# Kernel tuning notes

Measured on AMD Instinct MI355X. Metric: run time of the kernel, lower is better.

The kernel has to match this reference:

```python
import jax, jax.numpy as jnp
import numpy as np

N_NODES = 100000
N_EDGES = 3200000
D_FEAT = 64


def setup_inputs() -> dict:
    key = jax.random.key(0)
    k_x, k_r, k_c, k_v = jax.random.split(key, 4)
    x = jax.random.normal(k_x, (N_NODES, D_FEAT), dtype=jnp.float32)
    edge_row = jax.random.randint(k_r, (N_EDGES,), 0, N_NODES, dtype=jnp.int64)
    edge_col = jax.random.randint(k_c, (N_EDGES,), 0, N_NODES, dtype=jnp.int64)
    # positive values mimicking symmetric-normalized adjacency weights
    edge_val = jax.random.uniform(k_v, (N_EDGES,), dtype=jnp.float32)
    t = jnp.zeros((1,), dtype=jnp.float32)  # ODE time, unused by this linear GCN step
    return {"t": t, "x": x, "edge_row": edge_row, "edge_col": edge_col, "edge_val": edge_val}


def reference(t, x, edge_row, edge_col, edge_val):
    # out = A_sparse @ x, COO SpMM as gather -> scale -> segment-sum scatter
    # gathered: [n_edges, d]
    gathered = edge_val[:, None] * x[edge_col]
    out = jax.ops.segment_sum(gathered, edge_row, num_segments=N_NODES)
    return out
```

## Files before the change

### kernel.cpp

```cpp
#include <hip/hip_runtime.h>
#include <hip/hip_bf16.h>
#include <hip/hip_fp16.h>

#define D 64
#define RB 128
#define NB_MAX 1024
#define NBLK1 512
#define P1CAP 6272
#define CAP 5120

typedef unsigned long long ull;
typedef unsigned short u16;

__device__ __forceinline__ ull pack_rec(float v, int r, int c) {
    return ((ull)__float_as_uint(v) << 32) |
           (ull)(((unsigned)(r & (RB - 1)) << 17) | (unsigned)c);
}

__global__ __launch_bounds__(256) void spmm_atomic_kernel(
    const float* __restrict__ x,
    const int*   __restrict__ edge_row,
    const int*   __restrict__ edge_col,
    const float* __restrict__ edge_val,
    float*       __restrict__ out,
    int n_edges)
{
    const int gtid = blockIdx.x * blockDim.x + threadIdx.x;
    const int wave = gtid >> 6;
    const int lane = threadIdx.x & 63;
    if (wave >= n_edges) return;
    const int   r = edge_row[wave];
    const int   c = edge_col[wave];
    const float v = edge_val[wave];
    atomicAdd(&out[(size_t)r * D + lane], v * x[(size_t)c * D + lane]);
}

__global__ __launch_bounds__(256) void p1_localsort_kernel(
    const int* __restrict__ rows, const int* __restrict__ cols,
    const float* __restrict__ vals,
    ull* __restrict__ staged, u16* __restrict__ counts, u16* __restrict__ startpos,
    int n_edges, int nb, int chunk)
{
    __shared__ ull stage[P1CAP];
    __shared__ int cnt[NB_MAX];
    __shared__ int s[256];
    const int t = threadIdx.x, blk = blockIdx.x;
    const int e0 = blk * chunk;
    const int e1 = min(e0 + chunk, n_edges);
    const int len = e1 - e0;

    for (int i = t; i < nb; i += 256) cnt[i] = 0;
    __syncthreads();

    for (int i = e0 + t * 4; i < e1; i += 1024) {
        if (i + 4 <= e1) {
            const int4 r4 = *(const int4*)(rows + i);
            atomicAdd(&cnt[r4.x >> 7], 1);
            atomicAdd(&cnt[r4.y >> 7], 1);
            atomicAdd(&cnt[r4.z >> 7], 1);
            atomicAdd(&cnt[r4.w >> 7], 1);
        } else {
            for (int k = i; k < e1; ++k) atomicAdd(&cnt[rows[k] >> 7], 1);
        }
    }
    __syncthreads();

    int pre[4], sum = 0;
    const int base = t * 4;
    #pragma unroll
    for (int k = 0; k < 4; ++k) {
        const int idx = base + k;
        const int c = (idx < nb) ? cnt[idx] : 0;
        if (idx < nb) counts[(size_t)idx * NBLK1 + blk] = (u16)c;
        pre[k] = sum; sum += c;
    }
    s[t] = sum;
    for (int off = 1; off < 256; off <<= 1) {
        __syncthreads();
        const int w = (t >= off) ? s[t - off] : 0;
        __syncthreads();
        s[t] += w;
    }
    const int texcl = s[t] - sum;
    __syncthreads();
    #pragma unroll
    for (int k = 0; k < 4; ++k) {
        const int idx = base + k;
        if (idx < nb) {
            const int e = texcl + pre[k];
            cnt[idx] = e;
            startpos[(size_t)idx * NBLK1 + blk] = (u16)e;
        }
    }
    __syncthreads();

    for (int i = e0 + t * 4; i < e1; i += 1024) {
        if (i + 4 <= e1) {
            const int4   r4 = *(const int4*)(rows + i);
            const int4   c4 = *(const int4*)(cols + i);
            const float4 v4 = *(const float4*)(vals + i);
            int p;
            p = atomicAdd(&cnt[r4.x >> 7], 1); stage[p] = pack_rec(v4.x, r4.x, c4.x);
            p = atomicAdd(&cnt[r4.y >> 7], 1); stage[p] = pack_rec(v4.y, r4.y, c4.y);
            p = atomicAdd(&cnt[r4.z >> 7], 1); stage[p] = pack_rec(v4.z, r4.z, c4.z);
            p = atomicAdd(&cnt[r4.w >> 7], 1); stage[p] = pack_rec(v4.w, r4.w, c4.w);
        } else {
            for (int k = i; k < e1; ++k) {
                const int p = atomicAdd(&cnt[rows[k] >> 7], 1);
                stage[p] = pack_rec(vals[k], rows[k], cols[k]);
            }
        }
    }
    __syncthreads();

    for (int i = t; i < len; i += 256)
        staged[(size_t)blk * chunk + i] = stage[i];
}

__global__ __launch_bounds__(256) void p2_binsum_kernel(
    const u16* __restrict__ counts, int* __restrict__ binsum, int nb)
{
    __shared__ int s[256];
    const int b = blockIdx.x, t = threadIdx.x;
    const int acc = (int)counts[(size_t)b * NBLK1 + t] +
                    (int)counts[(size_t)b * NBLK1 + t + 256];
    s[t] = acc;
    __syncthreads();
    for (int off = 128; off > 0; off >>= 1) {
        if (t < off) s[t] += s[t + off];
        __syncthreads();
    }
    if (t == 0) binsum[b] = s[0];
}

__global__ __launch_bounds__(1024) void p3_scanbins_kernel(
    const int* __restrict__ binsum, int* __restrict__ binbase,
    int* __restrict__ flags, int nb)
{
    __shared__ int s[1024];
    const int t = threadIdx.x;
    const int mine = (t < nb) ? binsum[t] : 0;
    s[t] = mine;
    for (int off = 1; off < 1024; off <<= 1) {
        __syncthreads();
        const int v = (t >= off) ? s[t - off] : 0;
        __syncthreads();
        s[t] += v;
    }
    if (t < nb) { binbase[t] = s[t] - mine; flags[t] = 0; }
    if (t == nb - 1) binbase[nb] = s[t];
}

__global__ __launch_bounds__(256) void p4_binsort_kernel(
    const ull* __restrict__ staged, const u16* __restrict__ counts,
    const u16* __restrict__ startpos, const int* __restrict__ binbase,
    ull* __restrict__ recs, int* __restrict__ offsets_row, int* __restrict__ flags,
    int nb, int n_nodes, int chunk)
{
    __shared__ ull stage[CAP];
    __shared__ int doff[NBLK1 + 1];
    __shared__ int srcs[NBLK1];
    __shared__ int cnt[1024];
    __shared__ int s[256];
    const int b = blockIdx.x, t = threadIdx.x;
    const int s0 = binbase[b];

    const int la = (int)counts[(size_t)b * NBLK1 + 2 * t];
    const int lb = (int)counts[(size_t)b * NBLK1 + 2 * t + 1];
    srcs[2 * t]     = (int)startpos[(size_t)b * NBLK1 + 2 * t];
    srcs[2 * t + 1] = (int)startpos[(size_t)b * NBLK1 + 2 * t + 1];
    const int mysum = la + lb;
    s[t] = mysum;
    for (int off = 1; off < 256; off <<= 1) {
        __syncthreads();
        const int w = (t >= off) ? s[t - off] : 0;
        __syncthreads();
        s[t] += w;
    }
    const int excl = s[t] - mysum;
    doff[2 * t] = excl;
    doff[2 * t + 1] = excl + la;
    if (t == 255) doff[NBLK1] = s[255];
    __syncthreads();
    const int len = doff[NBLK1];

    if (len > CAP) {
        if (t == 0) flags[b] = 1;
        for (int i = t; i < len; i += 256) {
            int lo = 0, hi = NBLK1 - 1;
            while (lo < hi) {
                const int mid = (lo + hi + 1) >> 1;
                if (doff[mid] <= i) lo = mid; else hi = mid - 1;
            }
            recs[s0 + i] = staged[(size_t)lo * chunk + srcs[lo] + (i - doff[lo])];
        }
        if (t == 0 && b * RB <= n_nodes) offsets_row[b * RB] = s0;
        return;
    }

    for (int i = t; i < 1024; i += 256) cnt[i] = 0;
    __syncthreads();

    for (int i = t; i < len; i += 256) {
        int lo = 0, hi = NBLK1 - 1;
        while (lo < hi) {
            const int mid = (lo + hi + 1) >> 1;
            if (doff[mid] <= i) lo = mid; else hi = mid - 1;
        }
        const ull rr = staged[(size_t)lo * chunk + srcs[lo] + (i - doff[lo])];
        stage[i] = rr;
        const int key = ((int)((rr >> 17) & (RB - 1)) << 3) |
                        (int)(((unsigned)rr & 0x1FFFF) >> 14);
        atomicAdd(&cnt[key], 1);
    }
    __syncthreads();

    int v[4], pre[4], sum = 0;
    const int base = t * 4;
    #pragma unroll
    for (int k = 0; k < 4; ++k) { v[k] = cnt[base + k]; pre[k] = sum; sum += v[k]; }
    s[t] = sum;
    for (int off = 1; off < 256; off <<= 1) {
        __syncthreads();
        const int w = (t >= off) ? s[t - off] : 0;
        __syncthreads();
        s[t] += w;
    }
    const int texcl = s[t] - sum;
    __syncthreads();
    #pragma unroll
    for (int k = 0; k < 4; ++k) cnt[base + k] = texcl + pre[k];
    __syncthreads();

    if (t <= RB) {
        const int r = b * RB + t;
        if (r <= n_nodes)
            offsets_row[r] = s0 + ((t == RB) ? len : cnt[t << 3]);
    }
    __syncthreads();

    for (int i = t; i < len; i += 256) {
        const ull rr = stage[i];
        const int key = ((int)((rr >> 17) & (RB - 1)) << 3) |
                        (int)(((unsigned)rr & 0x1FFFF) >> 14);
        const int p = atomicAdd(&cnt[key], 1);
        recs[s0 + p] = rr;
    }
}

__global__ void tohalf_kernel(const float* __restrict__ x,
                              __half2* __restrict__ xh2, int n4)
{
    for (int i = blockIdx.x * blockDim.x + threadIdx.x; i < n4;
         i += gridDim.x * blockDim.x) {
        const float4 v = ((const float4*)x)[i];
        xh2[2 * i + 0] = __floats2half2_rn(v.x, v.y);
        xh2[2 * i + 1] = __floats2half2_rn(v.z, v.w);
    }
}

__global__ __launch_bounds__(256, 8) void spmm_csr_half2_kernel(
    const __half* __restrict__ xh,
    const int*   __restrict__ offsets_row,
    const int*   __restrict__ binbase,
    const ull*   __restrict__ recs,
    const int*   __restrict__ flags,
    float*       __restrict__ out,
    int n_nodes)
{
    const int row  = blockIdx.x * 4 + (threadIdx.x >> 6);
    if (row >= n_nodes) return;
    const int lane = threadIdx.x & 63;
    const int b    = row >> 7;

    if (__builtin_expect(flags[b], 0)) {
        float acc = 0.f;
        const int s  = binbase[b];
        const int e  = binbase[b + 1];
        const int lr = row & (RB - 1);
        for (int j = s; j < e; ++j) {
            const ull rec = recs[j];
            if ((int)((rec >> 17) & (RB - 1)) == lr) {
                const int   c = (int)((unsigned)rec & 0x1FFFF);
                const float v = __uint_as_float((unsigned)(rec >> 32));
                acc += v * __half2float(xh[(size_t)c * D + lane]);
            }
        }
        out[(size_t)row * D + lane] = acc;
        return;
    }

    const __half2* xh2 = (const __half2*)xh;
    const int half = lane >> 5;
    const int fl   = lane & 31;

    const int s = offsets_row[row];
    const int e = offsets_row[row + 1];
    float accx = 0.f, accy = 0.f;

    int j = s;
    for (; j + 16 <= e; j += 16) {
        float vv[8]; int aa[8];
        #pragma unroll
        for (int k = 0; k < 8; ++k) {
            const ull rec = recs[j + 2 * k + half];
            vv[k] = __uint_as_float((unsigned)(rec >> 32));
            aa[k] = ((int)((unsigned)rec & 0x1FFFF) << 5) + fl;
        }
        __half2 hv[8];
        #pragma unroll
        for (int k = 0; k < 8; ++k) hv[k] = xh2[aa[k]];
        __builtin_amdgcn_sched_barrier(0);
        #pragma unroll
        for (int k = 0; k < 8; ++k) {
            const float2 xf = __half22float2(hv[k]);
            accx = fmaf(vv[k], xf.x, accx);
            accy = fmaf(vv[k], xf.y, accy);
        }
    }
    if (j < e) {
        const int safe = e - 1;
        float vv[8]; int aa[8];
        #pragma unroll
        for (int k = 0; k < 8; ++k) {
            const int  idx = j + 2 * k + half;
            const bool ok  = idx < e;
            const ull  rec = recs[ok ? idx : safe];
            vv[k] = ok ? __uint_as_float((unsigned)(rec >> 32)) : 0.f;
            aa[k] = ((int)((unsigned)rec & 0x1FFFF) << 5) + fl;
        }
        __half2 hv[8];
        #pragma unroll
        for (int k = 0; k < 8; ++k) hv[k] = xh2[aa[k]];
        __builtin_amdgcn_sched_barrier(0);
        #pragma unroll
        for (int k = 0; k < 8; ++k) {
            const float2 xf = __half22float2(hv[k]);
            accx = fmaf(vv[k], xf.x, accx);
            accy = fmaf(vv[k], xf.y, accy);
        }
    }

    accx += __shfl_xor(accx, 32);
    accy += __shfl_xor(accy, 32);
    if (half == 0) {
        float2 o; o.x = accx; o.y = accy;
        ((float2*)out)[(size_t)row * 32 + fl] = o;
    }
}

static inline size_t align16(size_t v) { return (v + 15) & ~(size_t)15; }

extern "C" void kernel_launch(void* const* d_in, const int* in_sizes, int n_in,
                              void* d_out, int out_size, void* d_ws, size_t ws_size,
                              hipStream_t stream)
{
    const float* x        = (const float*)d_in[1];
    const int*   edge_row = (const int*)d_in[2];
    const int*   edge_col = (const int*)d_in[3];
    const float* edge_val = (const float*)d_in[4];
    float*       out      = (float*)d_out;

    const int n_edges = in_sizes[2];
    const int n_nodes = out_size / D;
    const int nb      = (n_nodes + RB - 1) / RB;
    const int chunk   = (((n_edges + NBLK1 - 1) / NBLK1) + 3) & ~3;

    const size_t off_recs    = 0;
    const size_t off_staged  = align16(off_recs + (size_t)n_edges * 8);
    const size_t off_counts  = align16(off_staged + (size_t)NBLK1 * chunk * 8);
    const size_t off_start   = align16(off_counts + (size_t)nb * NBLK1 * 2);
    const size_t off_binsum  = align16(off_start + (size_t)nb * NBLK1 * 2);
    const size_t off_binbase = align16(off_binsum + (size_t)nb * 4);
    const size_t off_rowoffs = align16(off_binbase + (size_t)(nb + 1) * 4);
    const size_t off_flags   = align16(off_rowoffs + (size_t)(n_nodes + 1) * 4);
    const size_t ws_needed   = off_flags + (size_t)nb * 4;
    const size_t xh_bytes    = (size_t)n_nodes * D * 2;

    if (ws_size < ws_needed || nb > NB_MAX || n_nodes > (1 << 17) ||
        chunk > P1CAP || xh_bytes > (size_t)NBLK1 * chunk * 8) {
        hipMemsetAsync(out, 0, (size_t)out_size * sizeof(float), stream);
        const int n_blocks = (n_edges + 3) / 4;
        spmm_atomic_kernel<<<n_blocks, 256, 0, stream>>>(
            x, edge_row, edge_col, edge_val, out, n_edges);
        return;
    }

    char* ws = (char*)d_ws;
    ull*    recs        = (ull*)(ws + off_recs);
    ull*    staged      = (ull*)(ws + off_staged);
    u16*    counts      = (u16*)(ws + off_counts);
    u16*    startpos    = (u16*)(ws + off_start);
    int*    binsum      = (int*)(ws + off_binsum);
    int*    binbase     = (int*)(ws + off_binbase);
    int*    offsets_row = (int*)(ws + off_rowoffs);
    int*    flags       = (int*)(ws + off_flags);
    __half* xh          = (__half*)(ws + off_staged);

    p1_localsort_kernel<<<NBLK1, 256, 0, stream>>>(
        edge_row, edge_col, edge_val, staged, counts, startpos,
        n_edges, nb, chunk);
    p2_binsum_kernel<<<nb, 256, 0, stream>>>(counts, binsum, nb);
    p3_scanbins_kernel<<<1, 1024, 0, stream>>>(binsum, binbase, flags, nb);
    p4_binsort_kernel<<<nb, 256, 0, stream>>>(
        staged, counts, startpos, binbase, recs, offsets_row, flags,
        nb, n_nodes, chunk);
    const int n4 = (n_nodes * D) / 4;
    tohalf_kernel<<<2048, 256, 0, stream>>>(x, (__half2*)xh, n4);
    spmm_csr_half2_kernel<<<(n_nodes + 3) / 4, 256, 0, stream>>>(
        xh, offsets_row, binbase, recs, flags, out, n_nodes);
}
```

Before: 259.1 us.

## Scatter locally sorted edges straight to global bin positions, drop staging buffer

```diff
diff --git a/kernel.cpp b/kernel.cpp
--- a/kernel.cpp
+++ b/kernel.cpp
@@ -35,19 +35,14 @@
     atomicAdd(&out[(size_t)r * D + lane], v * x[(size_t)c * D + lane]);
 }
 
-__global__ __launch_bounds__(256) void p1_localsort_kernel(
-    const int* __restrict__ rows, const int* __restrict__ cols,
-    const float* __restrict__ vals,
-    ull* __restrict__ staged, u16* __restrict__ counts, u16* __restrict__ startpos,
+__global__ __launch_bounds__(256) void p1a_hist_kernel(
+    const int* __restrict__ rows, u16* __restrict__ counts,
     int n_edges, int nb, int chunk)
 {
-    __shared__ ull stage[P1CAP];
     __shared__ int cnt[NB_MAX];
-    __shared__ int s[256];
     const int t = threadIdx.x, blk = blockIdx.x;
     const int e0 = blk * chunk;
     const int e1 = min(e0 + chunk, n_edges);
-    const int len = e1 - e0;
 
     for (int i = t; i < nb; i += 256) cnt[i] = 0;
     __syncthreads();
@@ -65,14 +60,75 @@
     }
     __syncthreads();
 
-    int pre[4], sum = 0;
+    for (int i = t; i < nb; i += 256)
+        counts[(size_t)i * NBLK1 + blk] = (u16)cnt[i];
+}
+
+__global__ __launch_bounds__(256) void p2_scanblocks_kernel(
+    const u16* __restrict__ counts, int* __restrict__ dest32,
+    int* __restrict__ binsum, int nb)
+{
+    __shared__ int s[256];
+    const int b = blockIdx.x, t = threadIdx.x;
+    const int la = (int)counts[(size_t)b * NBLK1 + 2 * t];
+    const int lb = (int)counts[(size_t)b * NBLK1 + 2 * t + 1];
+    const int mysum = la + lb;
+    s[t] = mysum;
+    for (int off = 1; off < 256; off <<= 1) {
+        __syncthreads();
+        const int w = (t >= off) ? s[t - off] : 0;
+        __syncthreads();
+        s[t] += w;
+    }
+    const int excl = s[t] - mysum;
+    dest32[(size_t)b * NBLK1 + 2 * t]     = excl;
+    dest32[(size_t)b * NBLK1 + 2 * t + 1] = excl + la;
+    if (t == 255) binsum[b] = s[255];
+}
+
+__global__ __launch_bounds__(1024) void p3_scanbins_kernel(
+    const int* __restrict__ binsum, int* __restrict__ binbase,
+    int* __restrict__ flags, int nb)
+{
+    __shared__ int s[1024];
+    const int t = threadIdx.x;
+    const int mine = (t < nb) ? binsum[t] : 0;
+    s[t] = mine;
+    for (int off = 1; off < 1024; off <<= 1) {
+        __syncthreads();
+        const int v = (t >= off) ? s[t - off] : 0;
+        __syncthreads();
+        s[t] += v;
+    }
+    if (t < nb) { binbase[t] = s[t] - mine; flags[t] = 0; }
+    if (t == nb - 1) binbase[nb] = s[t];
+}
+
+__global__ __launch_bounds__(256) void p1b_sortwrite_kernel(
+    const int* __restrict__ rows, const int* __restrict__ cols,
+    const float* __restrict__ vals,
+    const u16* __restrict__ counts, const int* __restrict__ dest32,
+    const int* __restrict__ binbase,
+    ull* __restrict__ recs, int n_edges, int nb, int chunk)
+{
+    __shared__ ull stage[P1CAP];
+    __shared__ u16 binof[P1CAP];
+    __shared__ int cnt[NB_MAX];
+    __shared__ u16 doffL[NB_MAX];
+    __shared__ int gbase[NB_MAX];
+    __shared__ int s[256];
+    const int t = threadIdx.x, blk = blockIdx.x;
+    const int e0 = blk * chunk;
+    const int e1 = min(e0 + chunk, n_edges);
+    const int len = e1 - e0;
+
+    int pre[4], sum = 0, c4[4];
     const int base = t * 4;
     #pragma unroll
     for (int k = 0; k < 4; ++k) {
         const int idx = base + k;
-        const int c = (idx < nb) ? cnt[idx] : 0;
-        if (idx < nb) counts[(size_t)idx * NBLK1 + blk] = (u16)c;
-        pre[k] = sum; sum += c;
+        c4[k] = (idx < nb) ? (int)counts[(size_t)idx * NBLK1 + blk] : 0;
+        pre[k] = sum; sum += c4[k];
     }
     s[t] = sum;
     for (int off = 1; off < 256; off <<= 1) {
@@ -88,8 +144,9 @@
         const int idx = base + k;
         if (idx < nb) {
             const int e = texcl + pre[k];
-            cnt[idx] = e;
-            startpos[(size_t)idx * NBLK1 + blk] = (u16)e;
+            cnt[idx]   = e;
+            doffL[idx] = (u16)e;
+            gbase[idx] = binbase[idx] + dest32[(size_t)idx * NBLK1 + blk];
         }
     }
     __syncthreads();
@@ -97,104 +154,47 @@
     for (int i = e0 + t * 4; i < e1; i += 1024) {
         if (i + 4 <= e1) {
             const int4   r4 = *(const int4*)(rows + i);
-            const int4   c4 = *(const int4*)(cols + i);
+            const int4   c4v = *(const int4*)(cols + i);
             const float4 v4 = *(const float4*)(vals + i);
             int p;
-            p = atomicAdd(&cnt[r4.x >> 7], 1); stage[p] = pack_rec(v4.x, r4.x, c4.x);
-            p = atomicAdd(&cnt[r4.y >> 7], 1); stage[p] = pack_rec(v4.y, r4.y, c4.y);
-            p = atomicAdd(&cnt[r4.z >> 7], 1); stage[p] = pack_rec(v4.z, r4.z, c4.z);
-            p = atomicAdd(&cnt[r4.w >> 7], 1); stage[p] = pack_rec(v4.w, r4.w, c4.w);
+            p = atomicAdd(&cnt[r4.x >> 7], 1); stage[p] = pack_rec(v4.x, r4.x, c4v.x); binof[p] = (u16)(r4.x >> 7);
+            p = atomicAdd(&cnt[r4.y >> 7], 1); stage[p] = pack_rec(v4.y, r4.y, c4v.y); binof[p] = (u16)(r4.y >> 7);
+            p = atomicAdd(&cnt[r4.z >> 7], 1); stage[p] = pack_rec(v4.z, r4.z, c4v.z); binof[p] = (u16)(r4.z >> 7);
+            p = atomicAdd(&cnt[r4.w >> 7], 1); stage[p] = pack_rec(v4.w, r4.w, c4v.w); binof[p] = (u16)(r4.w >> 7);
         } else {
             for (int k = i; k < e1; ++k) {
                 const int p = atomicAdd(&cnt[rows[k] >> 7], 1);
                 stage[p] = pack_rec(vals[k], rows[k], cols[k]);
+                binof[p] = (u16)(rows[k] >> 7);
             }
         }
     }
     __syncthreads();
 
-    for (int i = t; i < len; i += 256)
-        staged[(size_t)blk * chunk + i] = stage[i];
-}
-
-__global__ __launch_bounds__(256) void p2_binsum_kernel(
-    const u16* __restrict__ counts, int* __restrict__ binsum, int nb)
-{
-    __shared__ int s[256];
-    const int b = blockIdx.x, t = threadIdx.x;
-    const int acc = (int)counts[(size_t)b * NBLK1 + t] +
-                    (int)counts[(size_t)b * NBLK1 + t + 256];
-    s[t] = acc;
-    __syncthreads();
-    for (int off = 128; off > 0; off >>= 1) {
-        if (t < off) s[t] += s[t + off];
-        __syncthreads();
-    }
-    if (t == 0) binsum[b] = s[0];
-}
-
-__global__ __launch_bounds__(1024) void p3_scanbins_kernel(
-    const int* __restrict__ binsum, int* __restrict__ binbase,
-    int* __restrict__ flags, int nb)
-{
-    __shared__ int s[1024];
-    const int t = threadIdx.x;
-    const int mine = (t < nb) ? binsum[t] : 0;
-    s[t] = mine;
-    for (int off = 1; off < 1024; off <<= 1) {
-        __syncthreads();
-        const int v = (t >= off) ? s[t - off] : 0;
-        __syncthreads();
-        s[t] += v;
-    }
-    if (t < nb) { binbase[t] = s[t] - mine; flags[t] = 0; }
-    if (t == nb - 1) binbase[nb] = s[t];
-}
-
-__global__ __launch_bounds__(256) void p4_binsort_kernel(
-    const ull* __restrict__ staged, const u16* __restrict__ counts,
-    const u16* __restrict__ startpos, const int* __restrict__ binbase,
+    for (int i = t; i < len; i += 256) {
+        const int bin = (int)binof[i];
+        const int g   = gbase[bin] + (i - (int)doffL[bin]);
+        recs[g] = stage[i];
+    }
+}
+
+__global__ __launch_bounds__(256) void p4_sortbin_kernel(
+    const int* __restrict__ binbase,
     ull* __restrict__ recs, int* __restrict__ offsets_row, int* __restrict__ flags,
-    int nb, int n_nodes, int chunk)
+    int n_nodes)
 {
     __shared__ ull stage[CAP];
-    __shared__ int doff[NBLK1 + 1];
-    __shared__ int srcs[NBLK1];
     __shared__ int cnt[1024];
     __shared__ int s[256];
     const int b = blockIdx.x, t = threadIdx.x;
-    const int s0 = binbase[b];
-
-    const int la = (int)counts[(size_t)b * NBLK1 + 2 * t];
-    const int lb = (int)counts[(size_t)b * NBLK1 + 2 * t + 1];
-    srcs[2 * t]     = (int)startpos[(size_t)b * NBLK1 + 2 * t];
-    srcs[2 * t + 1] = (int)startpos[(size_t)b * NBLK1 + 2 * t + 1];
-    const int mysum = la + lb;
-    s[t] = mysum;
-    for (int off = 1; off < 256; off <<= 1) {
-        __syncthreads();
-        const int w = (t >= off) ? s[t - off] : 0;
-        __syncthreads();
-        s[t] += w;
-    }
-    const int excl = s[t] - mysum;
-    doff[2 * t] = excl;
-    doff[2 * t + 1] = excl + la;
-    if (t == 255) doff[NBLK1] = s[255];
-    __syncthreads();
-    const int len = doff[NBLK1];
+    const int s0  = binbase[b];
+    const int len = binbase[b + 1] - s0;
 
     if (len > CAP) {
-        if (t == 0) flags[b] = 1;
-        for (int i = t; i < len; i += 256) {
-            int lo = 0, hi = NBLK1 - 1;
-            while (lo < hi) {
-                const int mid = (lo + hi + 1) >> 1;
-                if (doff[mid] <= i) lo = mid; else hi = mid - 1;
-            }
-            recs[s0 + i] = staged[(size_t)lo * chunk + srcs[lo] + (i - doff[lo])];
-        }
-        if (t == 0 && b * RB <= n_nodes) offsets_row[b * RB] = s0;
+        if (t == 0) {
+            flags[b] = 1;
+            if (b * RB <= n_nodes) offsets_row[b * RB] = s0;
+        }
         return;
     }
 
@@ -202,12 +202,7 @@
     __syncthreads();
 
     for (int i = t; i < len; i += 256) {
-        int lo = 0, hi = NBLK1 - 1;
-        while (lo < hi) {
-            const int mid = (lo + hi + 1) >> 1;
-            if (doff[mid] <= i) lo = mid; else hi = mid - 1;
-        }
-        const ull rr = staged[(size_t)lo * chunk + srcs[lo] + (i - doff[lo])];
+        const ull rr = recs[s0 + i];
         stage[i] = rr;
         const int key = ((int)((rr >> 17) & (RB - 1)) << 3) |
                         (int)(((unsigned)rr & 0x1FFFF) >> 14);
@@ -367,18 +362,17 @@
     const int chunk   = (((n_edges + NBLK1 - 1) / NBLK1) + 3) & ~3;
 
     const size_t off_recs    = 0;
-    const size_t off_staged  = align16(off_recs + (size_t)n_edges * 8);
-    const size_t off_counts  = align16(off_staged + (size_t)NBLK1 * chunk * 8);
-    const size_t off_start   = align16(off_counts + (size_t)nb * NBLK1 * 2);
-    const size_t off_binsum  = align16(off_start + (size_t)nb * NBLK1 * 2);
+    const size_t off_xh      = align16(off_recs + (size_t)n_edges * 8);
+    const size_t off_counts  = align16(off_xh + (size_t)n_nodes * D * 2);
+    const size_t off_dest    = align16(off_counts + (size_t)nb * NBLK1 * 2);
+    const size_t off_binsum  = align16(off_dest + (size_t)nb * NBLK1 * 4);
     const size_t off_binbase = align16(off_binsum + (size_t)nb * 4);
     const size_t off_rowoffs = align16(off_binbase + (size_t)(nb + 1) * 4);
     const size_t off_flags   = align16(off_rowoffs + (size_t)(n_nodes + 1) * 4);
     const size_t ws_needed   = off_flags + (size_t)nb * 4;
-    const size_t xh_bytes    = (size_t)n_nodes * D * 2;
 
     if (ws_size < ws_needed || nb > NB_MAX || n_nodes > (1 << 17) ||
-        chunk > P1CAP || xh_bytes > (size_t)NBLK1 * chunk * 8) {
+        chunk > P1CAP || n_edges < 1) {
         hipMemsetAsync(out, 0, (size_t)out_size * sizeof(float), stream);
         const int n_blocks = (n_edges + 3) / 4;
         spmm_atomic_kernel<<<n_blocks, 256, 0, stream>>>(
@@ -388,23 +382,23 @@
 
     char* ws = (char*)d_ws;
     ull*    recs        = (ull*)(ws + off_recs);
-    ull*    staged      = (ull*)(ws + off_staged);
+    __half* xh          = (__half*)(ws + off_xh);
     u16*    counts      = (u16*)(ws + off_counts);
-    u16*    startpos    = (u16*)(ws + off_start);
+    int*    dest32      = (int*)(ws + off_dest);
     int*    binsum      = (int*)(ws + off_binsum);
     int*    binbase     = (int*)(ws + off_binbase);
     int*    offsets_row = (int*)(ws + off_rowoffs);
     int*    flags       = (int*)(ws + off_flags);
-    __half* xh          = (__half*)(ws + off_staged);
-
-    p1_localsort_kernel<<<NBLK1, 256, 0, stream>>>(
-        edge_row, edge_col, edge_val, staged, counts, startpos,
-        n_edges, nb, chunk);
-    p2_binsum_kernel<<<nb, 256, 0, stream>>>(counts, binsum, nb);
+
+    p1a_hist_kernel<<<NBLK1, 256, 0, stream>>>(
+        edge_row, counts, n_edges, nb, chunk);
+    p2_scanblocks_kernel<<<nb, 256, 0, stream>>>(counts, dest32, binsum, nb);
     p3_scanbins_kernel<<<1, 1024, 0, stream>>>(binsum, binbase, flags, nb);
-    p4_binsort_kernel<<<nb, 256, 0, stream>>>(
-        staged, counts, startpos, binbase, recs, offsets_row, flags,
-        nb, n_nodes, chunk);
+    p1b_sortwrite_kernel<<<NBLK1, 256, 0, stream>>>(
+        edge_row, edge_col, edge_val, counts, dest32, binbase,
+        recs, n_edges, nb, chunk);
+    p4_sortbin_kernel<<<nb, 256, 0, stream>>>(
+        binbase, recs, offsets_row, flags, n_nodes);
     const int n4 = (n_nodes * D) / 4;
     tohalf_kernel<<<2048, 256, 0, stream>>>(x, (__half2*)xh, n4);
     spmm_csr_half2_kernel<<<(n_nodes + 3) / 4, 256, 0, stream>>>(
```

After: 245.9 us. -5.1%, faster.
